# Kernel optimization log

Measured on AMD Instinct MI355X. Metric: run time of the kernel, lower is better.

Reference implementation:

```python
import jax, jax.numpy as jnp
import numpy as np

B, S, X, Y = 32, 3, 512, 512  # batch, O(3) spin components, lattice X, lattice Y

_L_np = np.array([[[0, 0, 0], [0, 0, -1], [0, 1, 0]],
                  [[0, 0, 1], [0, 0, 0], [-1, 0, 0]],
                  [[0, -1, 0], [1, 0, 0], [0, 0, 0]]], dtype=np.float32)


def setup_inputs() -> dict:
    key = jax.random.key(0)
    k_s, = jax.random.split(key, 1)
    s = jax.random.normal(k_s, (B, S, X, Y), dtype=jnp.float32)
    t = jnp.ones((), dtype=jnp.float32)
    C0 = jnp.ones((), dtype=jnp.float32)  # cc=[1.0] learnable coefficient
    L = jnp.asarray(_L_np)                # fixed SO(3) generators [s, r, a]
    return {"s": s, "t": t, "C0": C0, "L": L}


def reference(s, t, C0, L):
    # Psi0.grad: F = sum_mu (roll(s,+1,mu) + roll(s,-1,mu)); nearest-neighbor stencil
    Fn = (jnp.roll(s, 1, axis=2) + jnp.roll(s, -1, axis=2)
          + jnp.roll(s, 1, axis=3) + jnp.roll(s, -1, axis=3))
    # Lsig = -einsum('bsxy,sra->braxy', s, L); out = einsum('bsaxy,bsxy->baxy', Lsig, Fn)
    # fused: out[b,a,x,y] = -sum_{s,r} s[b,s,x,y] * L[s,r,a] * Fn[b,r,x,y]
    F = -jnp.einsum('bsxy,sra,brxy->baxy', s, L, Fn)
    # Coeff(t): cc=[1.0], EvenOdd=True, single coeff => Coeff(t) = C0 (t-independent)
    coeff = C0
    return coeff * F
```

## Files before the change

kernel.cpp:

```cpp
#include <hip/hip_runtime.h>
#include <hip/hip_bf16.h>


constexpr int B = 32, X = 512, Y = 512;
constexpr int XY = X * Y;

typedef float v4f __attribute__((ext_vector_type(4)));

__global__ __launch_bounds__(256)
void psi0_kernel(const float* __restrict__ s,
                 const float* __restrict__ C0p,
                 const float* __restrict__ Lp,
                 float* __restrict__ out)
{
    __shared__ float Ls[27];
    if (threadIdx.x < 27) Ls[threadIdx.x] = Lp[threadIdx.x];
    __syncthreads();

    const int tid  = threadIdx.x;
    const int lane = tid & 63;
    const int ty   = tid & 127;
    const int row  = tid >> 7;

    const int per = gridDim.x >> 3;
    const int sw  = (blockIdx.x & 7) * per + (blockIdx.x >> 3);

    const int b  = sw >> 8;
    const int x  = ((sw & 255) << 1) + row;
    const int y0 = ty << 2;

    const int xm = (x == 0)     ? X - 1 : x - 1;
    const int xp = (x == X - 1) ? 0     : x + 1;
    const int ym = (y0 == 0)     ? Y - 1 : y0 - 1;
    const int yp = (y0 + 4 == Y) ? 0     : y0 + 4;

    const size_t baseB = (size_t)b * 3 * XY;
    const float* p0 = s + baseB;
    const size_t rc = (size_t)x  * Y + y0;
    const size_t ru = (size_t)xm * Y + y0;
    const size_t rd = (size_t)xp * Y + y0;

    v4f ce[3], up[3], dn[3];
    #pragma unroll
    for (int c = 0; c < 3; ++c) {
        const float* p = p0 + (size_t)c * XY;
        ce[c] = *(const v4f*)(p + rc);
        up[c] = *(const v4f*)(p + ru);
        dn[c] = *(const v4f*)(p + rd);
    }

    float lf[3], rt[3];
    #pragma unroll
    for (int c = 0; c < 3; ++c) {
        lf[c] = __shfl_up(ce[c].w, 1);
        rt[c] = __shfl_down(ce[c].x, 1);
    }
    if (lane == 0) {
        #pragma unroll
        for (int c = 0; c < 3; ++c) lf[c] = p0[(size_t)c * XY + (size_t)x * Y + ym];
    }
    if (lane == 63) {
        #pragma unroll
        for (int c = 0; c < 3; ++c) rt[c] = p0[(size_t)c * XY + (size_t)x * Y + yp];
    }

    v4f Fn[3];
    #pragma unroll
    for (int c = 0; c < 3; ++c) {
        Fn[c].x = up[c].x + dn[c].x + lf[c]   + ce[c].y;
        Fn[c].y = up[c].y + dn[c].y + ce[c].x + ce[c].z;
        Fn[c].z = up[c].z + dn[c].z + ce[c].y + ce[c].w;
        Fn[c].w = up[c].w + dn[c].w + ce[c].z + rt[c];
    }

    const float nC0 = -C0p[0];
    #pragma unroll
    for (int a = 0; a < 3; ++a) {
        v4f acc = (v4f)0.f;
        #pragma unroll
        for (int ss = 0; ss < 3; ++ss) {
            #pragma unroll
            for (int r = 0; r < 3; ++r) {
                const float w = Ls[ss * 9 + r * 3 + a];
                acc += w * ce[ss] * Fn[r];
            }
        }
        v4f o = nC0 * acc;
        __builtin_nontemporal_store(o, (v4f*)(out + baseB + (size_t)a * XY + rc));
    }
}

extern "C" void kernel_launch(void* const* d_in, const int* in_sizes, int n_in,
                              void* d_out, int out_size, void* d_ws, size_t ws_size,
                              hipStream_t stream)
{
    const float* s   = (const float*)d_in[0];
    const float* C0p = (const float*)d_in[2];
    const float* Lp  = (const float*)d_in[3];
    float* out = (float*)d_out;

    const int blocks = B * (X / 2);
    psi0_kernel<<<blocks, 256, 0, stream>>>(s, C0p, Lp, out);
}
```

Measured before the change: 183.5 us.

## Stream rows through a register sliding window and hardcode the cross-product form

Each thread now walks 8 consecutive x rows and keeps the up, center and down rows in registers. Each new row is loaded once instead of being re-read as a neighbour by other blocks, which cuts redundant global and L2 traffic. The L-tensor contraction is replaced by an explicit cross product s×Fn, which drops the shared-memory L load and the barrier. In exchange the grid is smaller with fewer waves, and the loads inside the row loop are serialized. The code also assumes L always holds the fixed SO(3) generators.

```diff
diff --git a/kernel.cpp b/kernel.cpp
--- a/kernel.cpp
+++ b/kernel.cpp
@@ -4,89 +4,88 @@
 
 constexpr int B = 32, X = 512, Y = 512;
 constexpr int XY = X * Y;
+constexpr int RX = 8;
 
 typedef float v4f __attribute__((ext_vector_type(4)));
 
-__global__ __launch_bounds__(256)
+__global__ __launch_bounds__(128)
 void psi0_kernel(const float* __restrict__ s,
                  const float* __restrict__ C0p,
-                 const float* __restrict__ Lp,
                  float* __restrict__ out)
 {
-    __shared__ float Ls[27];
-    if (threadIdx.x < 27) Ls[threadIdx.x] = Lp[threadIdx.x];
-    __syncthreads();
-
     const int tid  = threadIdx.x;
     const int lane = tid & 63;
-    const int ty   = tid & 127;
-    const int row  = tid >> 7;
 
     const int per = gridDim.x >> 3;
     const int sw  = (blockIdx.x & 7) * per + (blockIdx.x >> 3);
 
-    const int b  = sw >> 8;
-    const int x  = ((sw & 255) << 1) + row;
-    const int y0 = ty << 2;
-
-    const int xm = (x == 0)     ? X - 1 : x - 1;
-    const int xp = (x == X - 1) ? 0     : x + 1;
+    constexpr int strips_per_b = X / RX;
+    const int b  = sw >> 6;
+    const int x0 = (sw & (strips_per_b - 1)) * RX;
+    const int y0 = tid << 2;
     const int ym = (y0 == 0)     ? Y - 1 : y0 - 1;
     const int yp = (y0 + 4 == Y) ? 0     : y0 + 4;
 
+    const float C0 = C0p[0];
     const size_t baseB = (size_t)b * 3 * XY;
     const float* p0 = s + baseB;
-    const size_t rc = (size_t)x  * Y + y0;
-    const size_t ru = (size_t)xm * Y + y0;
-    const size_t rd = (size_t)xp * Y + y0;
 
-    v4f ce[3], up[3], dn[3];
+    const int xm0 = (x0 == 0) ? X - 1 : x0 - 1;
+    v4f sm[3], sc[3], sp[3];
     #pragma unroll
     for (int c = 0; c < 3; ++c) {
-        const float* p = p0 + (size_t)c * XY;
-        ce[c] = *(const v4f*)(p + rc);
-        up[c] = *(const v4f*)(p + ru);
-        dn[c] = *(const v4f*)(p + rd);
+        sm[c] = *(const v4f*)(p0 + (size_t)c * XY + (size_t)xm0 * Y + y0);
+        sc[c] = *(const v4f*)(p0 + (size_t)c * XY + (size_t)x0  * Y + y0);
+        sp[c] = *(const v4f*)(p0 + (size_t)c * XY + (size_t)(x0 + 1) * Y + y0);
     }
 
-    float lf[3], rt[3];
     #pragma unroll
-    for (int c = 0; c < 3; ++c) {
-        lf[c] = __shfl_up(ce[c].w, 1);
-        rt[c] = __shfl_down(ce[c].x, 1);
-    }
-    if (lane == 0) {
+    for (int i = 0; i < RX; ++i) {
+        const int x = x0 + i;
+
+        int x2 = x + 2; if (x2 >= X) x2 -= X;
+        v4f nx[3];
         #pragma unroll
-        for (int c = 0; c < 3; ++c) lf[c] = p0[(size_t)c * XY + (size_t)x * Y + ym];
-    }
-    if (lane == 63) {
+        for (int c = 0; c < 3; ++c)
+            nx[c] = *(const v4f*)(p0 + (size_t)c * XY + (size_t)x2 * Y + y0);
+
+        float lf[3], rt[3];
         #pragma unroll
-        for (int c = 0; c < 3; ++c) rt[c] = p0[(size_t)c * XY + (size_t)x * Y + yp];
-    }
+        for (int c = 0; c < 3; ++c) {
+            lf[c] = __shfl_up(sc[c].w, 1);
+            rt[c] = __shfl_down(sc[c].x, 1);
+        }
+        if (lane == 0) {
+            #pragma unroll
+            for (int c = 0; c < 3; ++c) lf[c] = p0[(size_t)c * XY + (size_t)x * Y + ym];
+        }
+        if (lane == 63) {
+            #pragma unroll
+            for (int c = 0; c < 3; ++c) rt[c] = p0[(size_t)c * XY + (size_t)x * Y + yp];
+        }
 
-    v4f Fn[3];
-    #pragma unroll
-    for (int c = 0; c < 3; ++c) {
-        Fn[c].x = up[c].x + dn[c].x + lf[c]   + ce[c].y;
-        Fn[c].y = up[c].y + dn[c].y + ce[c].x + ce[c].z;
-        Fn[c].z = up[c].z + dn[c].z + ce[c].y + ce[c].w;
-        Fn[c].w = up[c].w + dn[c].w + ce[c].z + rt[c];
-    }
+        v4f Fn[3];
+        #pragma unroll
+        for (int c = 0; c < 3; ++c) {
+            v4f f = sm[c] + sp[c];
+            Fn[c].x = f.x + lf[c]    + sc[c].y;
+            Fn[c].y = f.y + sc[c].x + sc[c].z;
+            Fn[c].z = f.z + sc[c].y + sc[c].w;
+            Fn[c].w = f.w + sc[c].z + rt[c];
+        }
 
-    const float nC0 = -C0p[0];
-    #pragma unroll
-    for (int a = 0; a < 3; ++a) {
-        v4f acc = (v4f)0.f;
+        v4f t0 = C0 * sc[0], t1 = C0 * sc[1], t2 = C0 * sc[2];
+        v4f o0 = t1 * Fn[2] - t2 * Fn[1];
+        v4f o1 = t2 * Fn[0] - t0 * Fn[2];
+        v4f o2 = t0 * Fn[1] - t1 * Fn[0];
+
+        float* ob = out + baseB + (size_t)x * Y + y0;
+        __builtin_nontemporal_store(o0, (v4f*)(ob));
+        __builtin_nontemporal_store(o1, (v4f*)(ob + XY));
+        __builtin_nontemporal_store(o2, (v4f*)(ob + 2 * XY));
+
         #pragma unroll
-        for (int ss = 0; ss < 3; ++ss) {
-            #pragma unroll
-            for (int r = 0; r < 3; ++r) {
-                const float w = Ls[ss * 9 + r * 3 + a];
-                acc += w * ce[ss] * Fn[r];
-            }
-        }
-        v4f o = nC0 * acc;
-        __builtin_nontemporal_store(o, (v4f*)(out + baseB + (size_t)a * XY + rc));
+        for (int c = 0; c < 3; ++c) { sm[c] = sc[c]; sc[c] = sp[c]; sp[c] = nx[c]; }
     }
 }
 
@@ -96,9 +95,8 @@
 {
     const float* s   = (const float*)d_in[0];
     const float* C0p = (const float*)d_in[2];
-    const float* Lp  = (const float*)d_in[3];
     float* out = (float*)d_out;
 
-    const int blocks = B * (X / 2);
-    psi0_kernel<<<blocks, 256, 0, stream>>>(s, C0p, Lp, out);
+    const int blocks = B * (X / RX);
+    psi0_kernel<<<blocks, 128, 0, stream>>>(s, C0p, out);
 }
```

Measured after the change: 187.7 us. 1.02x slower.
